# Performance work log

Hardware: AMD Instinct MI355X
Metric: run time of the kernel (lower is better)

## Reference

```python
import math
import jax, jax.numpy as jnp
import numpy as np

B, T, D, K, H, L = 16384, 64, 32, 32, 32, 16
EPS = 1e-5

def _dct_basis(num_basis, horizon):
    # Type-II DCT rows, L2-normalized (matches build_dct_basis)
    n = np.arange(horizon, dtype=np.float32)
    rows = []
    for k in range(num_basis):
        if k == 0:
            rows.append(np.ones(horizon, dtype=np.float32) / math.sqrt(horizon))
        else:
            rows.append(np.sqrt(2.0 / horizon) * np.cos(math.pi * k * (2 * n + 1) / (2 * horizon)).astype(np.float32))
    return np.stack(rows, axis=0)

def setup_inputs() -> dict:
    key = jax.random.key(0)
    ks = jax.random.split(key, 6)
    sample = jax.random.normal(ks[0], (B, T, D), dtype=jnp.float32)
    basis = jnp.asarray(_dct_basis(K, T))                      # [K, T] learnable param, DCT init
    # Stacked per-basis MLP weights (K independent Linear(D,H)->GELU->Linear(H,L))
    W1 = jax.random.uniform(ks[1], (K, D, H), jnp.float32, -1.0, 1.0) / math.sqrt(D)
    b1 = jax.random.uniform(ks[2], (K, H), jnp.float32, -1.0, 1.0) / math.sqrt(D)
    W2 = jax.random.uniform(ks[3], (K, H, L), jnp.float32, -1.0, 1.0) / math.sqrt(H)
    b2 = jax.random.uniform(ks[4], (K, L), jnp.float32, -1.0, 1.0) / math.sqrt(H)
    gamma = jnp.ones((L,), jnp.float32)
    beta = jnp.zeros((L,), jnp.float32)
    return {"sample": sample, "basis": basis, "W1": W1, "b1": b1,
            "W2": W2, "b2": b2, "gamma": gamma, "beta": beta}

def reference(sample, basis, W1, b1, W2, b2, gamma, beta):
    # spectral projection: [B,K,D]
    coeffs = jnp.einsum('kt,btd->bkd', basis, sample)
    # K independent MLPs as one grouped GEMM (block-diagonal view of the ModuleList loop)
    h = jax.nn.gelu(jnp.einsum('bkd,kdh->bkh', coeffs, W1) + b1[None], approximate=False)
    z = jnp.einsum('bkh,khl->bkl', h, W2) + b2[None]           # [B,K,L]
    # LayerNorm over last dim
    mu = jnp.mean(z, axis=-1, keepdims=True)
    var = jnp.mean(jnp.square(z - mu), axis=-1, keepdims=True)
    return gamma * (z - mu) / jnp.sqrt(var + EPS) + beta
```

## Files before the change

### kernel.cpp

```cpp
#include <hip/hip_runtime.h>
#include <hip/hip_bf16.h>
#include <math.h>

#define B_TOT 16384
#define T_DIM 64
#define D_DIM 32
#define K_DIM 32
#define H_DIM 32
#define L_DIM 16
#define KBD (B_TOT * D_DIM)

__global__ void prep_transpose(const float* __restrict__ basis, float* __restrict__ basisT) {
    int i = blockIdx.x * blockDim.x + threadIdx.x;
    if (i < K_DIM * T_DIM) {
        int k = i / T_DIM, t = i % T_DIM;
        basisT[t * K_DIM + k] = basis[i];
    }
}

__global__ __launch_bounds__(256) void proj_kernel(const float* __restrict__ sample,
                                                   const float* __restrict__ basisT,
                                                   __hip_bfloat16* __restrict__ coeffs) {
    const int tid = threadIdx.x;
    const int bi = tid >> 5, d = tid & 31;
    const long b = (long)blockIdx.x * 8 + bi;

    float acc[K_DIM];
#pragma unroll
    for (int k = 0; k < K_DIM; ++k) acc[k] = 0.f;

    const float* sp = sample + b * (T_DIM * D_DIM) + d;
#pragma unroll 2
    for (int t = 0; t < T_DIM; ++t) {
        float sv = sp[t * D_DIM];
        const float* bt = basisT + t * K_DIM;
#pragma unroll
        for (int k = 0; k < K_DIM; ++k) acc[k] = fmaf(bt[k], sv, acc[k]);
    }

    __hip_bfloat16* cp = coeffs + b * D_DIM + d;
#pragma unroll
    for (int k = 0; k < K_DIM; ++k) cp[(long)k * KBD] = __float2bfloat16(acc[k]);
}

__device__ __forceinline__ float gelu_exact(float x) {
    const float iSqrt2 = 0.70710678118654752f;
    float y = x * iSqrt2;
    float ay = fabsf(y);
    float t = __builtin_amdgcn_rcpf(fmaf(0.3275911f, ay, 1.0f));
    float p = fmaf(fmaf(fmaf(fmaf(1.061405429f, t, -1.453152027f),
                             t, 1.421413741f),
                        t, -0.284496736f),
                   t, 0.254829592f) * t;
    float e = 1.0f - p * __expf(-ay * ay);
    e = copysignf(e, y);
    return 0.5f * x * (1.0f + e);
}

__global__ __launch_bounds__(256) void mlp_kernel(const __hip_bfloat16* __restrict__ coeffs,
                                                  const float* __restrict__ W1,
                                                  const float* __restrict__ b1,
                                                  const float* __restrict__ W2,
                                                  const float* __restrict__ b2,
                                                  const float* __restrict__ gamma,
                                                  const float* __restrict__ beta,
                                                  float* __restrict__ out) {
    const int tid = threadIdx.x;
    const int k = blockIdx.x >> 6;
    const long b = (long)(blockIdx.x & 63) * 256 + tid;

    const uint4* cp4 = reinterpret_cast<const uint4*>(coeffs + (long)k * KBD + b * D_DIM);
    float cv[D_DIM];
#pragma unroll
    for (int q = 0; q < 4; ++q) {
        uint4 u = cp4[q];
        unsigned int uu[4] = {u.x, u.y, u.z, u.w};
#pragma unroll
        for (int j = 0; j < 4; ++j) {
            cv[q * 8 + j * 2 + 0] = __uint_as_float(uu[j] << 16);
            cv[q * 8 + j * 2 + 1] = __uint_as_float(uu[j] & 0xffff0000u);
        }
    }

    const float* w1p = W1 + k * (D_DIM * H_DIM);
    const float* b1p = b1 + k * H_DIM;
    float h[H_DIM];
#pragma unroll
    for (int j = 0; j < H_DIM; ++j) h[j] = b1p[j];
#pragma unroll 4
    for (int d = 0; d < D_DIM; ++d) {
        const float* wr = w1p + d * H_DIM;
        float c = cv[d];
#pragma unroll
        for (int j = 0; j < H_DIM; ++j) h[j] = fmaf(c, wr[j], h[j]);
    }

#pragma unroll
    for (int j = 0; j < H_DIM; ++j) h[j] = gelu_exact(h[j]);

    const float* w2p = W2 + k * (H_DIM * L_DIM);
    const float* b2p = b2 + k * L_DIM;
    float z[L_DIM];
#pragma unroll
    for (int l = 0; l < L_DIM; ++l) z[l] = b2p[l];
#pragma unroll 4
    for (int hh = 0; hh < H_DIM; ++hh) {
        const float* wr = w2p + hh * L_DIM;
        float hv = h[hh];
#pragma unroll
        for (int l = 0; l < L_DIM; ++l) z[l] = fmaf(hv, wr[l], z[l]);
    }

    float mu = 0.f;
#pragma unroll
    for (int l = 0; l < L_DIM; ++l) mu += z[l];
    mu *= (1.0f / L_DIM);
    float var = 0.f;
#pragma unroll
    for (int l = 0; l < L_DIM; ++l) { float dz = z[l] - mu; var = fmaf(dz, dz, var); }
    var *= (1.0f / L_DIM);
    float rstd = rsqrtf(var + 1e-5f);

    float4 o[4];
    float* of = reinterpret_cast<float*>(o);
#pragma unroll
    for (int l = 0; l < L_DIM; ++l) of[l] = fmaf(gamma[l] * rstd, z[l] - mu, beta[l]);

    float4* op = reinterpret_cast<float4*>(out + (b * K_DIM + k) * L_DIM);
#pragma unroll
    for (int q = 0; q < 4; ++q) op[q] = o[q];
}

extern "C" void kernel_launch(void* const* d_in, const int* in_sizes, int n_in,
                              void* d_out, int out_size, void* d_ws, size_t ws_size,
                              hipStream_t stream) {
    const float* sample = (const float*)d_in[0];
    const float* basis  = (const float*)d_in[1];
    const float* W1     = (const float*)d_in[2];
    const float* b1     = (const float*)d_in[3];
    const float* W2     = (const float*)d_in[4];
    const float* b2     = (const float*)d_in[5];
    const float* gamma  = (const float*)d_in[6];
    const float* beta   = (const float*)d_in[7];
    float* out = (float*)d_out;

    float* basisT = (float*)d_ws;
    __hip_bfloat16* coeffs = (__hip_bfloat16*)((char*)d_ws + 32768);

    prep_transpose<<<8, 256, 0, stream>>>(basis, basisT);
    proj_kernel<<<B_TOT / 8, 256, 0, stream>>>(sample, basisT, coeffs);
    mlp_kernel<<<(B_TOT / 256) * K_DIM, 256, 0, stream>>>(coeffs, W1, b1, W2, b2, gamma, beta, out);
}
```

Baseline: 266.7 us.

## Fuse spectral projection and per-basis MLP into one kernel via LDS staging

```diff
diff --git a/kernel.cpp b/kernel.cpp
--- a/kernel.cpp
+++ b/kernel.cpp
@@ -8,7 +8,9 @@
 #define K_DIM 32
 #define H_DIM 32
 #define L_DIM 16
-#define KBD (B_TOT * D_DIM)
+#define NB 64
+#define NDP 16
+#define LDSB 17
 
 __global__ void prep_transpose(const float* __restrict__ basis, float* __restrict__ basisT) {
     int i = blockIdx.x * blockDim.x + threadIdx.x;
@@ -18,34 +20,14 @@
     }
 }
 
-__global__ __launch_bounds__(256) void proj_kernel(const float* __restrict__ sample,
-                                                   const float* __restrict__ basisT,
-                                                   __hip_bfloat16* __restrict__ coeffs) {
-    const int tid = threadIdx.x;
-    const int bi = tid >> 5, d = tid & 31;
-    const long b = (long)blockIdx.x * 8 + bi;
-
-    float acc[K_DIM];
-#pragma unroll
-    for (int k = 0; k < K_DIM; ++k) acc[k] = 0.f;
-
-    const float* sp = sample + b * (T_DIM * D_DIM) + d;
-#pragma unroll 2
-    for (int t = 0; t < T_DIM; ++t) {
-        float sv = sp[t * D_DIM];
-        const float* bt = basisT + t * K_DIM;
-#pragma unroll
-        for (int k = 0; k < K_DIM; ++k) acc[k] = fmaf(bt[k], sv, acc[k]);
-    }
-
-    __hip_bfloat16* cp = coeffs + b * D_DIM + d;
-#pragma unroll
-    for (int k = 0; k < K_DIM; ++k) cp[(long)k * KBD] = __float2bfloat16(acc[k]);
+__device__ __forceinline__ unsigned bf16_rne(float x) {
+    unsigned r = __float_as_uint(x);
+    r += 0x7fffu + ((r >> 16) & 1u);
+    return r >> 16;
 }
 
 __device__ __forceinline__ float gelu_exact(float x) {
-    const float iSqrt2 = 0.70710678118654752f;
-    float y = x * iSqrt2;
+    float y = x * 0.70710678118654752f;
     float ay = fabsf(y);
     float t = __builtin_amdgcn_rcpf(fmaf(0.3275911f, ay, 1.0f));
     float p = fmaf(fmaf(fmaf(fmaf(1.061405429f, t, -1.453152027f),
@@ -57,78 +39,110 @@
     return 0.5f * x * (1.0f + e);
 }
 
-__global__ __launch_bounds__(256) void mlp_kernel(const __hip_bfloat16* __restrict__ coeffs,
-                                                  const float* __restrict__ W1,
-                                                  const float* __restrict__ b1,
-                                                  const float* __restrict__ W2,
-                                                  const float* __restrict__ b2,
-                                                  const float* __restrict__ gamma,
-                                                  const float* __restrict__ beta,
-                                                  float* __restrict__ out) {
+__global__ __launch_bounds__(1024) void fused_kernel(const float* __restrict__ sample,
+                                                     const float* __restrict__ basisT,
+                                                     const float* __restrict__ W1,
+                                                     const float* __restrict__ b1,
+                                                     const float* __restrict__ W2,
+                                                     const float* __restrict__ b2,
+                                                     const float* __restrict__ gamma,
+                                                     const float* __restrict__ beta,
+                                                     float* __restrict__ out) {
+    __shared__ unsigned clds[K_DIM][NB][LDSB];
     const int tid = threadIdx.x;
-    const int k = blockIdx.x >> 6;
-    const long b = (long)(blockIdx.x & 63) * 256 + tid;
 
-    const uint4* cp4 = reinterpret_cast<const uint4*>(coeffs + (long)k * KBD + b * D_DIM);
-    float cv[D_DIM];
+    {
+        const int bl = tid >> 4;
+        const int dp = tid & 15;
+        const long b = (long)blockIdx.x * NB + bl;
+
+        float ax[K_DIM], ay[K_DIM];
 #pragma unroll
-    for (int q = 0; q < 4; ++q) {
-        uint4 u = cp4[q];
-        unsigned int uu[4] = {u.x, u.y, u.z, u.w};
+        for (int k = 0; k < K_DIM; ++k) { ax[k] = 0.f; ay[k] = 0.f; }
+
+        const float2* sp = reinterpret_cast<const float2*>(sample + b * (T_DIM * D_DIM)) + dp;
+#pragma unroll 4
+        for (int t = 0; t < T_DIM; ++t) {
+            float2 sv = sp[t * NDP];
+            const float* bt = basisT + t * K_DIM;
 #pragma unroll
-        for (int j = 0; j < 4; ++j) {
-            cv[q * 8 + j * 2 + 0] = __uint_as_float(uu[j] << 16);
-            cv[q * 8 + j * 2 + 1] = __uint_as_float(uu[j] & 0xffff0000u);
+            for (int k = 0; k < K_DIM; ++k) {
+                ax[k] = fmaf(bt[k], sv.x, ax[k]);
+                ay[k] = fmaf(bt[k], sv.y, ay[k]);
+            }
+        }
+#pragma unroll
+        for (int k = 0; k < K_DIM; ++k)
+            clds[k][bl][dp] = bf16_rne(ax[k]) | (bf16_rne(ay[k]) << 16);
+    }
+    __syncthreads();
+
+    {
+        const int w = tid >> 6;
+        const int lane = tid & 63;
+        const long b = (long)blockIdx.x * NB + lane;
+
+#pragma unroll 1
+        for (int rep = 0; rep < 2; ++rep) {
+            const int k = __builtin_amdgcn_readfirstlane(w + rep * 16);
+
+            float cv[D_DIM];
+#pragma unroll
+            for (int dp = 0; dp < NDP; ++dp) {
+                unsigned u = clds[k][lane][dp];
+                cv[2 * dp]     = __uint_as_float(u << 16);
+                cv[2 * dp + 1] = __uint_as_float(u & 0xffff0000u);
+            }
+
+            const float* w1p = W1 + k * (D_DIM * H_DIM);
+            const float* b1p = b1 + k * H_DIM;
+            float h[H_DIM];
+#pragma unroll
+            for (int j = 0; j < H_DIM; ++j) h[j] = b1p[j];
+#pragma unroll 4
+            for (int d = 0; d < D_DIM; ++d) {
+                const float* wr = w1p + d * H_DIM;
+                float c = cv[d];
+#pragma unroll
+                for (int j = 0; j < H_DIM; ++j) h[j] = fmaf(c, wr[j], h[j]);
+            }
+
+#pragma unroll
+            for (int j = 0; j < H_DIM; ++j) h[j] = gelu_exact(h[j]);
+
+            const float* w2p = W2 + k * (H_DIM * L_DIM);
+            const float* b2p = b2 + k * L_DIM;
+            float z[L_DIM];
+#pragma unroll
+            for (int l = 0; l < L_DIM; ++l) z[l] = b2p[l];
+#pragma unroll 4
+            for (int hh = 0; hh < H_DIM; ++hh) {
+                const float* wr = w2p + hh * L_DIM;
+                float hv = h[hh];
+#pragma unroll
+                for (int l = 0; l < L_DIM; ++l) z[l] = fmaf(hv, wr[l], z[l]);
+            }
+
+            float mu = 0.f;
+#pragma unroll
+            for (int l = 0; l < L_DIM; ++l) mu += z[l];
+            mu *= (1.0f / L_DIM);
+            float var = 0.f;
+#pragma unroll
+            for (int l = 0; l < L_DIM; ++l) { float dz = z[l] - mu; var = fmaf(dz, dz, var); }
+            var *= (1.0f / L_DIM);
+            float rstd = rsqrtf(var + 1e-5f);
+
+            float4 o[4];
+            float* of = reinterpret_cast<float*>(o);
+#pragma unroll
+            for (int l = 0; l < L_DIM; ++l) of[l] = fmaf(gamma[l] * rstd, z[l] - mu, beta[l]);
+
+            float4* op = reinterpret_cast<float4*>(out + (b * K_DIM + k) * L_DIM);
+#pragma unroll
+            for (int q = 0; q < 4; ++q) op[q] = o[q];
         }
     }
-
-    const float* w1p = W1 + k * (D_DIM * H_DIM);
-    const float* b1p = b1 + k * H_DIM;
-    float h[H_DIM];
-#pragma unroll
-    for (int j = 0; j < H_DIM; ++j) h[j] = b1p[j];
-#pragma unroll 4
-    for (int d = 0; d < D_DIM; ++d) {
-        const float* wr = w1p + d * H_DIM;
-        float c = cv[d];
-#pragma unroll
-        for (int j = 0; j < H_DIM; ++j) h[j] = fmaf(c, wr[j], h[j]);
-    }
-
-#pragma unroll
-    for (int j = 0; j < H_DIM; ++j) h[j] = gelu_exact(h[j]);
-
-    const float* w2p = W2 + k * (H_DIM * L_DIM);
-    const float* b2p = b2 + k * L_DIM;
-    float z[L_DIM];
-#pragma unroll
-    for (int l = 0; l < L_DIM; ++l) z[l] = b2p[l];
-#pragma unroll 4
-    for (int hh = 0; hh < H_DIM; ++hh) {
-        const float* wr = w2p + hh * L_DIM;
-        float hv = h[hh];
-#pragma unroll
-        for (int l = 0; l < L_DIM; ++l) z[l] = fmaf(hv, wr[l], z[l]);
-    }
-
-    float mu = 0.f;
-#pragma unroll
-    for (int l = 0; l < L_DIM; ++l) mu += z[l];
-    mu *= (1.0f / L_DIM);
-    float var = 0.f;
-#pragma unroll
-    for (int l = 0; l < L_DIM; ++l) { float dz = z[l] - mu; var = fmaf(dz, dz, var); }
-    var *= (1.0f / L_DIM);
-    float rstd = rsqrtf(var + 1e-5f);
-
-    float4 o[4];
-    float* of = reinterpret_cast<float*>(o);
-#pragma unroll
-    for (int l = 0; l < L_DIM; ++l) of[l] = fmaf(gamma[l] * rstd, z[l] - mu, beta[l]);
-
-    float4* op = reinterpret_cast<float4*>(out + (b * K_DIM + k) * L_DIM);
-#pragma unroll
-    for (int q = 0; q < 4; ++q) op[q] = o[q];
 }
 
 extern "C" void kernel_launch(void* const* d_in, const int* in_sizes, int n_in,
@@ -145,9 +159,8 @@
     float* out = (float*)d_out;
 
     float* basisT = (float*)d_ws;
-    __hip_bfloat16* coeffs = (__hip_bfloat16*)((char*)d_ws + 32768);
 
     prep_transpose<<<8, 256, 0, stream>>>(basis, basisT);
-    proj_kernel<<<B_TOT / 8, 256, 0, stream>>>(sample, basisT, coeffs);
-    mlp_kernel<<<(B_TOT / 256) * K_DIM, 256, 0, stream>>>(coeffs, W1, b1, W2, b2, gamma, beta, out);
+    fused_kernel<<<B_TOT / NB, 1024, 0, stream>>>(sample, basisT, W1, b1, W2, b2,
+                                                  gamma, beta, out);
 }
```

After: 279.1 us. +4.7%, slower.
